# Kernel optimization log

Measured on AMD Instinct MI355X. Metric: run time of the kernel, lower is better.

The kernel has to match this reference:

```python
import jax, jax.numpy as jnp
import numpy as np

B, S, IN, H, C = 4, 1024, 1024, 256, 8

def setup_inputs() -> dict:
    key = jax.random.key(0)
    ks = jax.random.split(key, 9)
    scale_in = 1.0 / np.sqrt(IN)
    scale_h2 = 1.0 / np.sqrt(2 * H)
    return {
        "seq_feats": jax.random.normal(ks[0], (B, S, IN), dtype=jnp.float32),
        "U": jax.random.normal(ks[1], (H, C, H), dtype=jnp.float32) * 0.02,
        "W_weight": jax.random.uniform(ks[2], (C, 2 * H), minval=-scale_h2, maxval=scale_h2, dtype=jnp.float32),
        "W_bias": jax.random.uniform(ks[3], (C,), minval=-scale_h2, maxval=scale_h2, dtype=jnp.float32),
        "start_w": jax.random.uniform(ks[4], (H, IN), minval=-scale_in, maxval=scale_in, dtype=jnp.float32),
        "start_b": jax.random.uniform(ks[5], (H,), minval=-scale_in, maxval=scale_in, dtype=jnp.float32),
        "end_w": jax.random.uniform(ks[6], (H, IN), minval=-scale_in, maxval=scale_in, dtype=jnp.float32),
        "end_b": jax.random.uniform(ks[7], (H,), minval=-scale_in, maxval=scale_in, dtype=jnp.float32),
    }

def reference(seq_feats, U, W_weight, W_bias, start_w, start_b, end_w, end_b):
    # Hs, He: [b, s, h]
    Hs = jnp.einsum('bsi,hi->bsh', seq_feats, start_w) + start_b
    He = jnp.einsum('bsi,hi->bsh', seq_feats, end_w) + end_b
    # biaffine: [b, s, e, c]
    biaff = jnp.einsum('bsh,hcg,beg->bsec', Hs, U, He)
    # Linear over concat([Hs_repeat, He_repeat]) == split-weight broadcast sum
    Ws, We = W_weight[:, :256], W_weight[:, 256:]
    lin = (jnp.einsum('bsh,ch->bsc', Hs, Ws)[:, :, None, :]
           + jnp.einsum('beh,ch->bec', He, We)[:, None, :, :]
           + W_bias)
    return biaff + lin
```

## Files before the change

kernel.cpp:

```cpp
#include <hip/hip_runtime.h>
#include <stdint.h>


#define BDIM 256

typedef float f32x4 __attribute__((ext_vector_type(4)));
typedef __bf16 bf16x8 __attribute__((ext_vector_type(8)));
typedef unsigned int u32;
typedef unsigned short u16;
typedef const __attribute__((address_space(1))) u32* gas_ptr;
typedef __attribute__((address_space(3))) u32* las_ptr;

static __device__ __forceinline__ void load_lds16(const void* g, void* l) {
  __builtin_amdgcn_global_load_lds((gas_ptr)g, (las_ptr)l, 16, 0, 0);
}

static __device__ __forceinline__ u16 f32_to_bf16(float f) {
  union { float f; u32 u; } v; v.f = f;
  u32 r = v.u + 0x7FFFu + ((v.u >> 16) & 1u);
  return (u16)(r >> 16);
}
static __device__ __forceinline__ u32 pack_bf16(float lo, float hi) {
  return (u32)f32_to_bf16(lo) | ((u32)f32_to_bf16(hi) << 16);
}
static __device__ __forceinline__ float bf16lo_to_f32(u32 u) {
  union { u32 u; float f; } v; v.u = u << 16;
  return v.f;
}
static __device__ __forceinline__ float bf16hi_to_f32(u32 u) {
  union { u32 u; float f; } v; v.u = u & 0xFFFF0000u;
  return v.f;
}

static __device__ __forceinline__ void stage32(u16* lds, int dst, const u16* src,
                                               int srow, int ld, int kcol, int tid) {
  const int r = tid >> 3;
  const int sl = tid & 7;
  load_lds16(src + (size_t)(srow + r) * ld + kcol + ((sl ^ (r & 7)) << 3),
             &lds[dst + tid * 8]);
}

static __device__ __forceinline__ void stage32_f32(u16* lds, int dst, const float* src,
                                                   int srow, int ld, int kcol, int tid) {
  const int r = tid >> 3;
  const int sl = tid & 7;
  const float* p = src + (size_t)(srow + r) * ld + kcol + ((sl ^ (r & 7)) << 3);
  const float4 v0 = *reinterpret_cast<const float4*>(p);
  const float4 v1 = *reinterpret_cast<const float4*>(p + 4);
  uint4 w;
  w.x = pack_bf16(v0.x, v0.y);
  w.y = pack_bf16(v0.z, v0.w);
  w.z = pack_bf16(v1.x, v1.y);
  w.w = pack_bf16(v1.z, v1.w);
  *reinterpret_cast<uint4*>(&lds[dst + tid * 8]) = w;
}

static __device__ __forceinline__ bf16x8 rd64(const u16* lds, int base, int row, int kslot) {
  return *reinterpret_cast<const bf16x8*>(&lds[base + row * 64 + ((kslot ^ (row & 7)) << 3)]);
}

__global__ __launch_bounds__(BDIM, 4)
void k1p(const float* __restrict__ seq,
         const float* __restrict__ sw,
         const float* __restrict__ ew,
         const float* __restrict__ U,
         const float* __restrict__ sb,
         const float* __restrict__ eb,
         u16* __restrict__ Hboth,
         u16* __restrict__ Ut)
{
  const int tid = threadIdx.x;
  const int bid = blockIdx.x;

  if (bid >= 512) {
    const int i = (bid - 512) * 1024 + tid * 4;
    const int n = i >> 8;
    const int h = i & 255;
    ushort4 o;
    o.x = f32_to_bf16(U[(size_t)(h + 0) * 2048 + n]);
    o.y = f32_to_bf16(U[(size_t)(h + 1) * 2048 + n]);
    o.z = f32_to_bf16(U[(size_t)(h + 2) * 2048 + n]);
    o.w = f32_to_bf16(U[(size_t)(h + 3) * 2048 + n]);
    *reinterpret_cast<ushort4*>(Ut + i) = o;
    return;
  }

  __shared__ u16 lds[2 * 4096];

  const int lane = tid & 63;
  const int wv   = tid >> 6;
  const int wr   = wv >> 1;
  const int wq   = wv & 1;
  const int rA   = lane & 15;
  const int kq   = lane >> 4;

  int id = bid;
  id = (id & 7) * 64 + (id >> 3);
  const int n0 = (id & 7) * 64;
  const int m0 = (id >> 3) * 64;

  const float* wsrc = (n0 < 256) ? (sw + (size_t)n0 * 1024)
                                 : (ew + (size_t)(n0 - 256) * 1024);

  f32x4 acc[2][2];
#pragma unroll
  for (int i = 0; i < 2; ++i)
#pragma unroll
    for (int j = 0; j < 2; ++j) acc[i][j] = (f32x4)0.f;

#pragma unroll 1
  for (int kt = 0; kt < 1024; kt += 64) {
    stage32_f32(lds, 0,           seq,  m0,      1024, kt, tid);
    stage32_f32(lds, 2048,        seq,  m0 + 32, 1024, kt, tid);
    stage32_f32(lds, 4096,        wsrc, 0,       1024, kt, tid);
    stage32_f32(lds, 4096 + 2048, wsrc, 32,      1024, kt, tid);
    __syncthreads();

    bf16x8 aF[2][2], bF[2][2];
#pragma unroll
    for (int mi = 0; mi < 2; ++mi)
#pragma unroll
      for (int ks = 0; ks < 2; ++ks)
        aF[mi][ks] = rd64(lds, 0, wr * 32 + mi * 16 + rA, (ks << 2) | kq);
#pragma unroll
    for (int ni = 0; ni < 2; ++ni)
#pragma unroll
      for (int ks = 0; ks < 2; ++ks)
        bF[ni][ks] = rd64(lds, 4096, wq * 32 + ni * 16 + rA, (ks << 2) | kq);
#pragma unroll
    for (int mi = 0; mi < 2; ++mi)
#pragma unroll
      for (int ni = 0; ni < 2; ++ni)
#pragma unroll
        for (int ks = 0; ks < 2; ++ks)
          acc[mi][ni] = __builtin_amdgcn_mfma_f32_16x16x32_bf16(
              aF[mi][ks], bF[ni][ks], acc[mi][ni], 0, 0, 0);
    __syncthreads();
  }

#pragma unroll
  for (int mi = 0; mi < 2; ++mi) {
#pragma unroll
    for (int ni = 0; ni < 2; ++ni) {
      const int n = n0 + wq * 32 + ni * 16 + rA;
      const float bn = (n < 256) ? sb[n] : eb[n - 256];
      const int mr = m0 + wr * 32 + mi * 16 + kq * 4;
#pragma unroll
      for (int r = 0; r < 4; ++r)
        Hboth[(size_t)(mr + r) * 512 + n] = f32_to_bf16(acc[mi][ni][r] + bn);
    }
  }
}

__global__ __launch_bounds__(BDIM, 2)
void k2lin(const u16* __restrict__ Hboth,
           const u16* __restrict__ Utbf,
           u16* __restrict__ Tbf,
           const float* __restrict__ Ww,
           const float* __restrict__ Wb,
           float* __restrict__ linS,
           float* __restrict__ linE)
{
  const int bid = blockIdx.x;
  const int tid = threadIdx.x;

  if (bid >= 512) {
    const int idx = (bid - 512) * BDIM + tid;
    const int m = idx >> 3;
    const int c = idx & 7;
    const uint4* hs4 = reinterpret_cast<const uint4*>(Hboth + (size_t)m * 512);
    const uint4* he4 = reinterpret_cast<const uint4*>(Hboth + (size_t)m * 512 + 256);
    const float* wsp = Ww + c * 512;
    const float* wep = wsp + 256;
    float s1 = 0.f, s2 = 0.f;
#pragma unroll 4
    for (int t = 0; t < 32; ++t) {
      const uint4 a = hs4[t];
      const uint4 b = he4[t];
      const u32 aw[4] = {a.x, a.y, a.z, a.w};
      const u32 bw[4] = {b.x, b.y, b.z, b.w};
#pragma unroll
      for (int q = 0; q < 4; ++q) {
        const int h = t * 8 + q * 2;
        s1 += bf16lo_to_f32(aw[q]) * wsp[h] + bf16hi_to_f32(aw[q]) * wsp[h + 1];
        s2 += bf16lo_to_f32(bw[q]) * wep[h] + bf16hi_to_f32(bw[q]) * wep[h + 1];
      }
    }
    linS[idx] = s1;
    linE[idx] = s2 + Wb[c];
    return;
  }

  __shared__ u16 lds[2 * 8192];

  int id = bid;
  id = (id & 7) * 64 + (id >> 3);
  const int n0 = (id & 15) * 128;
  const int m0 = (id >> 4) * 128;

  const int lane = tid & 63;
  const int wv   = tid >> 6;
  const int wr   = wv >> 1;
  const int wc   = wv & 1;
  const int rA   = lane & 15;
  const int kq   = lane >> 4;

  f32x4 acc[4][4];
#pragma unroll
  for (int i = 0; i < 4; ++i)
#pragma unroll
    for (int j = 0; j < 4; ++j) acc[i][j] = (f32x4)0.f;

#pragma unroll 1
  for (int kt = 0; kt < 256; kt += 64) {
#pragma unroll
    for (int h = 0; h < 4; ++h)
      stage32(lds, h * 2048, Hboth, m0 + h * 32, 512, kt, tid);
#pragma unroll
    for (int h = 0; h < 4; ++h)
      stage32(lds, 8192 + h * 2048, Utbf, n0 + h * 32, 256, kt, tid);
    __syncthreads();

    bf16x8 aF[4][2], bF[4][2];
#pragma unroll
    for (int mi = 0; mi < 4; ++mi)
#pragma unroll
      for (int ks = 0; ks < 2; ++ks)
        aF[mi][ks] = rd64(lds, 0, wr * 64 + mi * 16 + rA, (ks << 2) | kq);
#pragma unroll
    for (int ni = 0; ni < 4; ++ni)
#pragma unroll
      for (int ks = 0; ks < 2; ++ks)
        bF[ni][ks] = rd64(lds, 8192, wc * 64 + ni * 16 + rA, (ks << 2) | kq);
#pragma unroll
    for (int mi = 0; mi < 4; ++mi)
#pragma unroll
      for (int ni = 0; ni < 4; ++ni)
#pragma unroll
        for (int ks = 0; ks < 2; ++ks)
          acc[mi][ni] = __builtin_amdgcn_mfma_f32_16x16x32_bf16(
              aF[mi][ks], bF[ni][ks], acc[mi][ni], 0, 0, 0);
    __syncthreads();
  }

#pragma unroll
  for (int mi = 0; mi < 4; ++mi) {
#pragma unroll
    for (int ni = 0; ni < 4; ++ni) {
      const int mBase = m0 + wr * 64 + mi * 16 + kq * 4;
      const int n = n0 + wc * 64 + ni * 16 + rA;
#pragma unroll
      for (int r = 0; r < 4; ++r)
        Tbf[(size_t)(mBase + r) * 2048 + n] = f32_to_bf16(acc[mi][ni][r]);
    }
  }
}

#define K3STAGE(buf, t) do {                                                   \
    _Pragma("unroll")                                                          \
    for (int h = 0; h < 4; ++h)                                                \
      stage32(lds, (buf) * 16384 + h * 2048, Ag, m0 + h * 32, 256, (t) * 64, tid); \
    _Pragma("unroll")                                                          \
    for (int h = 0; h < 4; ++h)                                                \
      stage32(lds, (buf) * 16384 + 8192 + h * 2048, Bgz, n0 + h * 32, 512, (t) * 64, tid); \
  } while (0)

__global__ __launch_bounds__(BDIM, 2)
void gemm128_biaff(const u16* __restrict__ Tall,
                   const u16* __restrict__ Bg,
                   float* __restrict__ Out,
                   const float* __restrict__ linSall,
                   const float* __restrict__ linEall)
{
  __shared__ u16 lds[4 * 8192];

  const int tid  = threadIdx.x;
  const int lane = tid & 63;
  const int wv   = tid >> 6;
  const int wr   = wv >> 1;
  const int wc   = wv & 1;
  const int rA   = lane & 15;
  const int kq   = lane >> 4;
  const int z    = blockIdx.z;

  int id = blockIdx.y * gridDim.x + blockIdx.x;
  id = (id & 7) * 64 + (id >> 3);
  const int n0 = (id & 7) * 128;
  const int m0 = (id >> 3) * 128;

  const u16* Ag  = Tall + (size_t)z * (8192 * 256);
  const u16* Bgz = Bg   + (size_t)z * (1024 * 512);

  f32x4 acc[4][4];
#pragma unroll
  for (int i = 0; i < 4; ++i)
#pragma unroll
    for (int j = 0; j < 4; ++j) acc[i][j] = (f32x4)0.f;

  const float* lS = linSall + (size_t)z * 8192;
  float4 ls4[4];
#pragma unroll
  for (int mi = 0; mi < 4; ++mi)
    ls4[mi] = *reinterpret_cast<const float4*>(lS + m0 + wr * 64 + mi * 16 + kq * 4);

  K3STAGE(0, 0);

#pragma unroll
  for (int t = 0; t < 4; ++t) {
    const int cur = t & 1;
    if (t < 3) {
      K3STAGE(cur ^ 1, t + 1);
      asm volatile("s_waitcnt vmcnt(8)" ::: "memory");
    } else {
      asm volatile("s_waitcnt vmcnt(0)" ::: "memory");
    }
    __builtin_amdgcn_sched_barrier(0);
    __builtin_amdgcn_s_barrier();

    bf16x8 aF[4][2], bF[4][2];
#pragma unroll
    for (int mi = 0; mi < 4; ++mi)
#pragma unroll
      for (int ks = 0; ks < 2; ++ks)
        aF[mi][ks] = rd64(lds, cur * 16384, wr * 64 + mi * 16 + rA, (ks << 2) | kq);
#pragma unroll
    for (int ni = 0; ni < 4; ++ni)
#pragma unroll
      for (int ks = 0; ks < 2; ++ks)
        bF[ni][ks] = rd64(lds, cur * 16384 + 8192, wc * 64 + ni * 16 + rA, (ks << 2) | kq);
#pragma unroll
    for (int mi = 0; mi < 4; ++mi)
#pragma unroll
      for (int ni = 0; ni < 4; ++ni)
#pragma unroll
        for (int ks = 0; ks < 2; ++ks)
          acc[mi][ni] = __builtin_amdgcn_mfma_f32_16x16x32_bf16(
              aF[mi][ks], bF[ni][ks], acc[mi][ni], 0, 0, 0);

    __builtin_amdgcn_sched_barrier(0);
    __builtin_amdgcn_s_barrier();
  }

  float* OutZ = Out + (size_t)z * 8388608;
  const float* lE = linEall + (size_t)z * 8192;
#pragma unroll
  for (int mi = 0; mi < 4; ++mi) {
#pragma unroll
    for (int ni = 0; ni < 4; ++ni) {
      const int mBase = m0 + wr * 64 + mi * 16 + kq * 4;
      const int e = n0 + wc * 64 + ni * 16 + rA;
      const int s = mBase >> 3;
      const int c0 = mBase & 7;
      const float4 le4 = *reinterpret_cast<const float4*>(lE + (e << 3) + c0);
      float4 o;
      o.x = acc[mi][ni][0] + ls4[mi].x + le4.x;
      o.y = acc[mi][ni][1] + ls4[mi].y + le4.y;
      o.z = acc[mi][ni][2] + ls4[mi].z + le4.z;
      o.w = acc[mi][ni][3] + ls4[mi].w + le4.w;
      *reinterpret_cast<float4*>(OutZ + ((size_t)s << 13) + ((size_t)e << 3) + c0) = o;
    }
  }
}

extern "C" void kernel_launch(void* const* d_in, const int* in_sizes, int n_in,
                              void* d_out, int out_size, void* d_ws, size_t ws_size,
                              hipStream_t stream)
{
  const float* seq = (const float*)d_in[0];
  const float* U   = (const float*)d_in[1];
  const float* Ww  = (const float*)d_in[2];
  const float* Wb  = (const float*)d_in[3];
  const float* sw  = (const float*)d_in[4];
  const float* sb  = (const float*)d_in[5];
  const float* ew  = (const float*)d_in[6];
  const float* eb  = (const float*)d_in[7];
  float* out = (float*)d_out;

  u16* Utbf  = (u16*)d_ws;
  u16* Hboth = Utbf + 524288;
  u16* Tbf   = Hboth + 2097152;
  float* linS = (float*)(Tbf + 8388608);
  float* linE = linS + 32768;

  k1p<<<1024, BDIM, 0, stream>>>(seq, sw, ew, U, sb, eb, Hboth, Utbf);

  k2lin<<<640, BDIM, 0, stream>>>(Hboth, Utbf, Tbf, Ww, Wb, linS, linE);

  gemm128_biaff<<<dim3(8, 64, 4), BDIM, 0, stream>>>(
      Tbf, Hboth + 256, out, linS, linE);
}
```

Measured before the change: 80.77 us.

## Software-pipeline k1p register prefetch and double-buffer k2lin LDS staging

Result: slower. 84.76 us (+4.9%).

```diff
diff --git a/kernel.cpp b/kernel.cpp
--- a/kernel.cpp
+++ b/kernel.cpp
@@ -40,23 +40,28 @@
              &lds[dst + tid * 8]);
 }
 
-static __device__ __forceinline__ void stage32_f32(u16* lds, int dst, const float* src,
-                                                   int srow, int ld, int kcol, int tid) {
+static __device__ __forceinline__ bf16x8 rd64(const u16* lds, int base, int row, int kslot) {
+  return *reinterpret_cast<const bf16x8*>(&lds[base + row * 64 + ((kslot ^ (row & 7)) << 3)]);
+}
+
+struct F8 { float4 a, b; };
+static __device__ __forceinline__ F8 ldf8(const float* src, int srow, int ld,
+                                          int kcol, int tid) {
   const int r = tid >> 3;
   const int sl = tid & 7;
   const float* p = src + (size_t)(srow + r) * ld + kcol + ((sl ^ (r & 7)) << 3);
-  const float4 v0 = *reinterpret_cast<const float4*>(p);
-  const float4 v1 = *reinterpret_cast<const float4*>(p + 4);
+  F8 v;
+  v.a = *reinterpret_cast<const float4*>(p);
+  v.b = *reinterpret_cast<const float4*>(p + 4);
+  return v;
+}
+static __device__ __forceinline__ void wrf8(u16* lds, int dst, F8 v, int tid) {
   uint4 w;
-  w.x = pack_bf16(v0.x, v0.y);
-  w.y = pack_bf16(v0.z, v0.w);
-  w.z = pack_bf16(v1.x, v1.y);
-  w.w = pack_bf16(v1.z, v1.w);
+  w.x = pack_bf16(v.a.x, v.a.y);
+  w.y = pack_bf16(v.a.z, v.a.w);
+  w.z = pack_bf16(v.b.x, v.b.y);
+  w.w = pack_bf16(v.b.z, v.b.w);
   *reinterpret_cast<uint4*>(&lds[dst + tid * 8]) = w;
-}
-
-static __device__ __forceinline__ bf16x8 rd64(const u16* lds, int base, int row, int kslot) {
-  return *reinterpret_cast<const bf16x8*>(&lds[base + row * 64 + ((kslot ^ (row & 7)) << 3)]);
 }
 
 __global__ __launch_bounds__(BDIM, 4)
@@ -108,13 +113,23 @@
 #pragma unroll
     for (int j = 0; j < 2; ++j) acc[i][j] = (f32x4)0.f;
 
+  F8 s0 = ldf8(seq,  m0,      1024, 0, tid);
+  F8 s1 = ldf8(seq,  m0 + 32, 1024, 0, tid);
+  F8 s2 = ldf8(wsrc, 0,       1024, 0, tid);
+  F8 s3 = ldf8(wsrc, 32,      1024, 0, tid);
+  wrf8(lds, 0, s0, tid); wrf8(lds, 2048, s1, tid);
+  wrf8(lds, 4096, s2, tid); wrf8(lds, 6144, s3, tid);
+  __syncthreads();
+
 #pragma unroll 1
-  for (int kt = 0; kt < 1024; kt += 64) {
-    stage32_f32(lds, 0,           seq,  m0,      1024, kt, tid);
-    stage32_f32(lds, 2048,        seq,  m0 + 32, 1024, kt, tid);
-    stage32_f32(lds, 4096,        wsrc, 0,       1024, kt, tid);
-    stage32_f32(lds, 4096 + 2048, wsrc, 32,      1024, kt, tid);
-    __syncthreads();
+  for (int t = 0; t < 16; ++t) {
+    if (t < 15) {
+      const int kc = (t + 1) * 64;
+      s0 = ldf8(seq,  m0,      1024, kc, tid);
+      s1 = ldf8(seq,  m0 + 32, 1024, kc, tid);
+      s2 = ldf8(wsrc, 0,       1024, kc, tid);
+      s3 = ldf8(wsrc, 32,      1024, kc, tid);
+    }
 
     bf16x8 aF[2][2], bF[2][2];
 #pragma unroll
@@ -136,6 +151,12 @@
           acc[mi][ni] = __builtin_amdgcn_mfma_f32_16x16x32_bf16(
               aF[mi][ks], bF[ni][ks], acc[mi][ni], 0, 0, 0);
     __syncthreads();
+
+    if (t < 15) {
+      wrf8(lds, 0, s0, tid); wrf8(lds, 2048, s1, tid);
+      wrf8(lds, 4096, s2, tid); wrf8(lds, 6144, s3, tid);
+    }
+    __syncthreads();
   }
 
 #pragma unroll
@@ -151,6 +172,15 @@
     }
   }
 }
+
+#define K2STAGE(buf, t) do {                                                   \
+    _Pragma("unroll")                                                          \
+    for (int h = 0; h < 4; ++h)                                                \
+      stage32(lds, (buf) * 16384 + h * 2048, Hboth, m0 + h * 32, 512, (t) * 64, tid); \
+    _Pragma("unroll")                                                          \
+    for (int h = 0; h < 4; ++h)                                                \
+      stage32(lds, (buf) * 16384 + 8192 + h * 2048, Utbf, n0 + h * 32, 256, (t) * 64, tid); \
+  } while (0)
 
 __global__ __launch_bounds__(BDIM, 2)
 void k2lin(const u16* __restrict__ Hboth,
@@ -191,7 +221,7 @@
     return;
   }
 
-  __shared__ u16 lds[2 * 8192];
+  __shared__ u16 lds[4 * 8192];
 
   int id = bid;
   id = (id & 7) * 64 + (id >> 3);
@@ -211,27 +241,31 @@
 #pragma unroll
     for (int j = 0; j < 4; ++j) acc[i][j] = (f32x4)0.f;
 
-#pragma unroll 1
-  for (int kt = 0; kt < 256; kt += 64) {
-#pragma unroll
-    for (int h = 0; h < 4; ++h)
-      stage32(lds, h * 2048, Hboth, m0 + h * 32, 512, kt, tid);
-#pragma unroll
-    for (int h = 0; h < 4; ++h)
-      stage32(lds, 8192 + h * 2048, Utbf, n0 + h * 32, 256, kt, tid);
-    __syncthreads();
+  K2STAGE(0, 0);
+
+#pragma unroll
+  for (int t = 0; t < 4; ++t) {
+    const int cur = t & 1;
+    if (t < 3) {
+      K2STAGE(cur ^ 1, t + 1);
+      asm volatile("s_waitcnt vmcnt(8)" ::: "memory");
+    } else {
+      asm volatile("s_waitcnt vmcnt(0)" ::: "memory");
+    }
+    __builtin_amdgcn_sched_barrier(0);
+    __builtin_amdgcn_s_barrier();
 
     bf16x8 aF[4][2], bF[4][2];
 #pragma unroll
     for (int mi = 0; mi < 4; ++mi)
 #pragma unroll
       for (int ks = 0; ks < 2; ++ks)
-        aF[mi][ks] = rd64(lds, 0, wr * 64 + mi * 16 + rA, (ks << 2) | kq);
+        aF[mi][ks] = rd64(lds, cur * 16384, wr * 64 + mi * 16 + rA, (ks << 2) | kq);
 #pragma unroll
     for (int ni = 0; ni < 4; ++ni)
 #pragma unroll
       for (int ks = 0; ks < 2; ++ks)
-        bF[ni][ks] = rd64(lds, 8192, wc * 64 + ni * 16 + rA, (ks << 2) | kq);
+        bF[ni][ks] = rd64(lds, cur * 16384 + 8192, wc * 64 + ni * 16 + rA, (ks << 2) | kq);
 #pragma unroll
     for (int mi = 0; mi < 4; ++mi)
 #pragma unroll
@@ -240,7 +274,9 @@
         for (int ks = 0; ks < 2; ++ks)
           acc[mi][ni] = __builtin_amdgcn_mfma_f32_16x16x32_bf16(
               aF[mi][ks], bF[ni][ks], acc[mi][ni], 0, 0, 0);
-    __syncthreads();
+
+    __builtin_amdgcn_sched_barrier(0);
+    __builtin_amdgcn_s_barrier();
   }
 
 #pragma unroll
```
